# Kernel optimization log

Measured on AMD Instinct MI355X. Metric: run time of the kernel, lower is better.

## Reference

```python
import jax, jax.numpy as jnp
import numpy as np

N, C, H = 4096, 1024, 16
HD = C // H            # 64
DR = HD // 8           # 8 rope freqs per spatial axis


def setup_inputs() -> dict:
    key = jax.random.key(0)
    k1, k2, k3, k4, k5, k6 = jax.random.split(key, 6)
    x = jax.random.normal(k1, (N, C), dtype=jnp.float32)
    coords = jax.random.randint(k2, (N, 5), 0, 64, dtype=jnp.int32)  # [batch, t, h, w, z]
    w_qkv = jax.random.normal(k3, (3 * C, C), dtype=jnp.float32) / np.sqrt(C)
    w_out = jax.random.normal(k4, (C, C), dtype=jnp.float32) / np.sqrt(C)
    gamma_q = jnp.ones((H, HD), dtype=jnp.float32)
    gamma_k = jnp.ones((H, HD), dtype=jnp.float32)
    return {"x": x, "coords": coords, "w_qkv": w_qkv, "w_out": w_out,
            "gamma_q": gamma_q, "gamma_k": gamma_k}


def _rms_norm(t, gamma):
    # F.normalize(dim=-1) * gamma * sqrt(head_dim), computed in fp32
    t = t.astype(jnp.float32)
    nrm = jnp.linalg.norm(t, axis=-1, keepdims=True)
    return t / jnp.maximum(nrm, 1e-12) * gamma * np.float32(np.sqrt(HD))


def _rope_angles(coords):
    # freqs = 1/10000^(arange(DR)/HD); angles per axis (t,h,w,z), concat -> [N, 4*DR] = [N, HD/2]
    freqs = 1.0 / (10000.0 ** (jnp.arange(DR, dtype=jnp.float32) / HD))
    pos = coords[:, 1:].astype(jnp.float32)  # [N,4]
    ang = pos[:, :, None] * freqs[None, None, :]  # [N,4,DR]
    return ang.reshape(ang.shape[0], -1)  # [N, HD/2]


def _apply_rope(t, cos, sin):
    # t: [N,H,HD]; pairs (2i, 2i+1) rotated by angle[i]
    t2 = t.astype(jnp.float32).reshape(t.shape[0], t.shape[1], -1, 2)
    re = t2[..., 0] * cos - t2[..., 1] * sin
    im = t2[..., 0] * sin + t2[..., 1] * cos
    return jnp.stack([re, im], axis=-1).reshape(t.shape)


def reference(x, coords, w_qkv, w_out, gamma_q, gamma_k):
    n = x.shape[0]
    qkv = (x @ w_qkv.T).reshape(n, 3, H, HD)
    q, k, v = qkv[:, 0], qkv[:, 1], qkv[:, 2]  # [N,H,HD]
    q = _rms_norm(q, gamma_q)
    k = _rms_norm(k, gamma_k)
    ang = _rope_angles(coords)              # [N, HD/2]
    cos = jnp.cos(ang)[:, None, :]          # [N,1,HD/2] (broadcast over heads)
    sin = jnp.sin(ang)[:, None, :]
    q = _apply_rope(q, cos, sin)
    k = _apply_rope(k, cos, sin)
    scale = np.float32(1.0 / np.sqrt(HD))
    scores = jnp.einsum('nhd,mhd->hnm', q, k) * scale  # [H,N,N]
    attn = jax.nn.softmax(scores, axis=-1)
    out = jnp.einsum('hnm,mhd->nhd', attn, v).reshape(n, C)
    return out @ w_out.T
```

## Files before the change

### kernel.cpp

```cpp
#include <hip/hip_runtime.h>
#include <hip/hip_bf16.h>

typedef _Float16 half8 __attribute__((ext_vector_type(8)));
typedef _Float16 half4v __attribute__((ext_vector_type(4)));
typedef _Float16 half2 __attribute__((ext_vector_type(2)));
typedef float f32x4 __attribute__((ext_vector_type(4)));

constexpr int NT = 4096;
constexpr int CH = 1024;
constexpr int NH = 16;
constexpr int HD = 64;
constexpr int C3 = 3072;

#if __has_builtin(__builtin_amdgcn_exp2f)
#define EXP2(x) __builtin_amdgcn_exp2f(x)
#else
#define EXP2(x) exp2f(x)
#endif

#define GLOAD_LDS16(gp, lp) __builtin_amdgcn_global_load_lds( \
    (const __attribute__((address_space(1))) void*)(gp),      \
    (__attribute__((address_space(3))) void*)(lp), 16, 0, 0)

static __device__ inline half2 pk_f16(float a, float b) {
  auto r = __builtin_amdgcn_cvt_pkrtz(a, b);
  return *(half2*)&r;
}

__global__ __launch_bounds__(256) void cvt_kernel(const float* __restrict__ in,
                                                  _Float16* __restrict__ out, int n4) {
  int i = blockIdx.x * 256 + threadIdx.x;
  if (i >= n4) return;
  float4 v = ((const float4*)in)[i];
  half4v h;
  h[0] = (_Float16)v.x; h[1] = (_Float16)v.y; h[2] = (_Float16)v.z; h[3] = (_Float16)v.w;
  ((half4v*)out)[i] = h;
}

template <typename OutT>
__global__ __launch_bounds__(256) void gemm_bt(const _Float16* __restrict__ A,
                                               const _Float16* __restrict__ Bt,
                                               OutT* __restrict__ Cc,
                                               int M, int Nn, int K) {
  __shared__ _Float16 As[128][32];
  __shared__ _Float16 Bs[128][32];
  const int tid = threadIdx.x;
  const int lane = tid & 63, w = tid >> 6;
  const int l15 = lane & 15, l4 = lane >> 4;
  const int m0 = blockIdx.x * 128, n0 = blockIdx.y * 128;
  const int wr = w >> 1, wc = w & 1;
  const int rb = w * 32;
  const int rl = lane >> 2;
  const int cb = (lane & 3) * 8;
  f32x4 acc[4][4] = {};
  for (int k0 = 0; k0 < K; k0 += 32) {
    __syncthreads();
    GLOAD_LDS16(A  + (size_t)(m0 + rb + rl) * K + k0 + cb,      &As[rb][0]);
    GLOAD_LDS16(A  + (size_t)(m0 + rb + 16 + rl) * K + k0 + cb, &As[rb + 16][0]);
    GLOAD_LDS16(Bt + (size_t)(n0 + rb + rl) * K + k0 + cb,      &Bs[rb][0]);
    GLOAD_LDS16(Bt + (size_t)(n0 + rb + 16 + rl) * K + k0 + cb, &Bs[rb + 16][0]);
    __syncthreads();
    half8 af[4], bf[4];
#pragma unroll
    for (int mt = 0; mt < 4; ++mt) af[mt] = *(half8*)&As[wr * 64 + mt * 16 + l15][l4 * 8];
#pragma unroll
    for (int nt = 0; nt < 4; ++nt) bf[nt] = *(half8*)&Bs[wc * 64 + nt * 16 + l15][l4 * 8];
#pragma unroll
    for (int mt = 0; mt < 4; ++mt)
#pragma unroll
      for (int nt = 0; nt < 4; ++nt)
        acc[mt][nt] = __builtin_amdgcn_mfma_f32_16x16x32_f16(af[mt], bf[nt], acc[mt][nt], 0, 0, 0);
  }
#pragma unroll
  for (int mt = 0; mt < 4; ++mt)
#pragma unroll
    for (int nt = 0; nt < 4; ++nt)
#pragma unroll
      for (int r = 0; r < 4; ++r) {
        int row = m0 + wr * 64 + mt * 16 + l4 * 4 + r;
        int col = n0 + wc * 64 + nt * 16 + l15;
        Cc[(size_t)row * Nn + col] = (OutT)acc[mt][nt][r];
      }
}

__global__ __launch_bounds__(256) void rmsrope_kernel(const _Float16* __restrict__ qkv,
                                                      const int* __restrict__ coords,
                                                      const float* __restrict__ gq,
                                                      const float* __restrict__ gk,
                                                      _Float16* __restrict__ Qh,
                                                      _Float16* __restrict__ KF) {
  int gw = blockIdx.x * 4 + (threadIdx.x >> 6);
  int lane = threadIdx.x & 63;
  int n = gw >> 4, h = gw & 15;
  float q = (float)qkv[(size_t)n * C3 + h * HD + lane];
  float k = (float)qkv[(size_t)n * C3 + CH + h * HD + lane];
  float sq = q * q, sk = k * k;
#pragma unroll
  for (int m = 1; m < 64; m <<= 1) { sq += __shfl_xor(sq, m); sk += __shfl_xor(sk, m); }
  q *= 8.0f / fmaxf(sqrtf(sq), 1e-12f) * gq[h * HD + lane];
  k *= 8.0f / fmaxf(sqrtf(sk), 1e-12f) * gk[h * HD + lane];
  int j = lane >> 1, p = j >> 3, dr = j & 7;
  float ang = (float)coords[n * 5 + 1 + p] * __expf(-(float)dr * 0.14391157f);
  float cs = cosf(ang), sn = sinf(ang);
  float qp = __shfl_xor(q, 1), kp = __shfl_xor(k, 1);
  float qr, kr;
  if ((lane & 1) == 0) { qr = q * cs - qp * sn; kr = k * cs - kp * sn; }
  else                 { qr = qp * sn + q * cs; kr = kp * sn + k * cs; }
  Qh[((size_t)h * NT + n) * HD + lane] = (_Float16)(qr * 0.18033688f);
  int m64 = n & 63, kb = n >> 6;
  int t   = 2 * (m64 >> 5) + ((m64 >> 2) & 1);
  int i15 = 4 * ((m64 >> 3) & 3) + (m64 & 3);
  int kk = lane >> 5, ll4 = (lane >> 3) & 3, jj = lane & 7;
  KF[(size_t)h * NT * HD + (size_t)kb * 4096 +
     (size_t)(((t * 2 + kk) * 64 + ll4 * 16 + i15) * 8 + jj)] = (_Float16)kr;
}

__global__ __launch_bounds__(256) void vtrans_kernel(const _Float16* __restrict__ qkv,
                                                     _Float16* __restrict__ VF) {
  __shared__ _Float16 L[64][72];
  int h = blockIdx.y, n0 = blockIdx.x * 64, kb = blockIdx.x, t0 = threadIdx.x;
#pragma unroll
  for (int i = 0; i < 2; ++i) {
    int cid = t0 + i * 256, r = cid >> 3, c = cid & 7;
    *(half8*)&L[r][c * 8] = *(const half8*)(qkv + (size_t)(n0 + r) * C3 + 2 * CH + h * HD + c * 8);
  }
  __syncthreads();
#pragma unroll
  for (int i = 0; i < 2; ++i) {
    int cid = t0 + i * 256, d = cid >> 3, c = cid & 7;
    half8 v;
#pragma unroll
    for (int jj = 0; jj < 8; ++jj) v[jj] = L[c * 8 + jj][d];
    size_t flat = (size_t)h * NT * HD + (size_t)kb * 4096 +
                  (size_t)((((d >> 4) * 2 + (c >> 2)) * 64 + (c & 3) * 16 + (d & 15)) * 8);
    *(half8*)(VF + flat) = v;
  }
}

__global__ __launch_bounds__(256, 2) void attn_kernel(const _Float16* __restrict__ Qh,
                                                      const _Float16* __restrict__ KF,
                                                      const _Float16* __restrict__ VF,
                                                      _Float16* __restrict__ Oh) {
  const int tid = threadIdx.x, lane = tid & 63, w = tid >> 6;
  const int l15 = lane & 15, l4 = lane >> 4;
  int bid = blockIdx.x;
  int s = bid >> 3;
  int h = (bid & 7) * 2 + (s >> 5);
  int n0 = (s & 31) * 128;
  half8 qf[2][2];
#pragma unroll
  for (int qb = 0; qb < 2; ++qb)
#pragma unroll
    for (int kk = 0; kk < 2; ++kk)
      qf[qb][kk] = *(const half8*)(Qh + ((size_t)h * NT + n0 + w * 32 + qb * 16 + l15) * HD + kk * 32 + l4 * 8);
  f32x4 acc[2][4] = {};
  f32x4 acc5[2] = {};
  half8 of1 = {};
  if (l15 == 0) {
#pragma unroll
    for (int jq = 0; jq < 8; ++jq) of1[jq] = (_Float16)1.0f;
  }
  const _Float16* KFb = KF + (size_t)h * NT * HD + lane * 8;
  const _Float16* VFb = VF + (size_t)h * NT * HD + lane * 8;
  half8 kA[8], vA[8], kB[8], vB[8];
  auto loadset = [&](int kb, half8 (&k)[8], half8 (&v)[8]) {
    const _Float16* kp = KFb + (size_t)kb * 4096;
    const _Float16* vp = VFb + (size_t)kb * 4096;
#pragma unroll
    for (int f = 0; f < 8; ++f) {
      k[f] = *(const half8*)(kp + f * 512);
      v[f] = *(const half8*)(vp + f * 512);
    }
  };
  auto compute = [&](half8 (&k)[8], half8 (&v)[8]) {
    f32x4 sv[2][4] = {};
    __builtin_amdgcn_s_setprio(1);
#pragma unroll
    for (int t = 0; t < 4; ++t)
#pragma unroll
      for (int kk = 0; kk < 2; ++kk) {
        sv[0][t] = __builtin_amdgcn_mfma_f32_16x16x32_f16(k[t * 2 + kk], qf[0][kk], sv[0][t], 0, 0, 0);
        sv[1][t] = __builtin_amdgcn_mfma_f32_16x16x32_f16(k[t * 2 + kk], qf[1][kk], sv[1][t], 0, 0, 0);
      }
    __builtin_amdgcn_s_setprio(0);
    union U { half8 v; half2 p[4]; };
    U u[2][2];
#pragma unroll
    for (int qb = 0; qb < 2; ++qb) {
      float e[4][4];
#pragma unroll
      for (int t = 0; t < 4; ++t)
#pragma unroll
        for (int r = 0; r < 4; ++r) e[t][r] = EXP2(sv[qb][t][r]);
      u[qb][0].p[0] = pk_f16(e[0][0], e[0][1]); u[qb][0].p[1] = pk_f16(e[0][2], e[0][3]);
      u[qb][0].p[2] = pk_f16(e[1][0], e[1][1]); u[qb][0].p[3] = pk_f16(e[1][2], e[1][3]);
      u[qb][1].p[0] = pk_f16(e[2][0], e[2][1]); u[qb][1].p[1] = pk_f16(e[2][2], e[2][3]);
      u[qb][1].p[2] = pk_f16(e[3][0], e[3][1]); u[qb][1].p[3] = pk_f16(e[3][2], e[3][3]);
    }
    __builtin_amdgcn_s_setprio(1);
#pragma unroll
    for (int t = 0; t < 4; ++t)
#pragma unroll
      for (int kk = 0; kk < 2; ++kk) {
        acc[0][t] = __builtin_amdgcn_mfma_f32_16x16x32_f16(u[0][kk].v, v[t * 2 + kk], acc[0][t], 0, 0, 0);
        acc[1][t] = __builtin_amdgcn_mfma_f32_16x16x32_f16(u[1][kk].v, v[t * 2 + kk], acc[1][t], 0, 0, 0);
      }
    acc5[0] = __builtin_amdgcn_mfma_f32_16x16x32_f16(u[0][0].v, of1, acc5[0], 0, 0, 0);
    acc5[0] = __builtin_amdgcn_mfma_f32_16x16x32_f16(u[0][1].v, of1, acc5[0], 0, 0, 0);
    acc5[1] = __builtin_amdgcn_mfma_f32_16x16x32_f16(u[1][0].v, of1, acc5[1], 0, 0, 0);
    acc5[1] = __builtin_amdgcn_mfma_f32_16x16x32_f16(u[1][1].v, of1, acc5[1], 0, 0, 0);
    __builtin_amdgcn_s_setprio(0);
  };
  loadset(0, kA, vA);
  for (int kb = 0; kb < 64; kb += 2) {
    loadset(kb + 1, kB, vB);
    compute(kA, vA);
    if (kb + 2 < 64) loadset(kb + 2, kA, vA);
    compute(kB, vB);
  }
#pragma unroll
  for (int qb = 0; qb < 2; ++qb) {
    float linv[4];
#pragma unroll
    for (int r = 0; r < 4; ++r) linv[r] = 1.0f / __shfl(acc5[qb][r], lane & 48);
#pragma unroll
    for (int t = 0; t < 4; ++t)
#pragma unroll
      for (int r = 0; r < 4; ++r) {
        int row = n0 + w * 32 + qb * 16 + l4 * 4 + r;
        Oh[(size_t)row * CH + h * HD + t * 16 + l15] = (_Float16)(acc[qb][t][r] * linv[r]);
      }
  }
}

extern "C" void kernel_launch(void* const* d_in, const int* in_sizes, int n_in,
                              void* d_out, int out_size, void* d_ws, size_t ws_size,
                              hipStream_t stream) {
  const float* x      = (const float*)d_in[0];
  const int*   coords = (const int*)d_in[1];
  const float* w_qkv  = (const float*)d_in[2];
  const float* w_out  = (const float*)d_in[3];
  const float* gq     = (const float*)d_in[4];
  const float* gk     = (const float*)d_in[5];
  float* out = (float*)d_out;

  char* ws = (char*)d_ws;
  size_t off = 0;
  auto alloc = [&](size_t bytes) { char* p = ws + off; off += bytes; return p; };
  _Float16* xh   = (_Float16*)alloc((size_t)NT * CH * 2);
  _Float16* wqh  = (_Float16*)alloc((size_t)C3 * CH * 2);
  _Float16* woh  = (_Float16*)alloc((size_t)CH * CH * 2);
  _Float16* qkvh = (_Float16*)alloc((size_t)NT * C3 * 2);
  _Float16* Qh   = (_Float16*)alloc((size_t)NT * CH * 2);
  _Float16* KFh  = (_Float16*)alloc((size_t)NT * CH * 2);
  _Float16* VFh  = (_Float16*)alloc((size_t)NT * CH * 2);
  _Float16* Oh   = (_Float16*)alloc((size_t)NT * CH * 2);
  if (off > ws_size) return;

  cvt_kernel<<<NT * CH / 4 / 256, 256, 0, stream>>>(x, xh, NT * CH / 4);
  cvt_kernel<<<C3 * CH / 4 / 256, 256, 0, stream>>>(w_qkv, wqh, C3 * CH / 4);
  cvt_kernel<<<CH * CH / 4 / 256, 256, 0, stream>>>(w_out, woh, CH * CH / 4);
  gemm_bt<_Float16><<<dim3(NT / 128, C3 / 128), 256, 0, stream>>>(xh, wqh, qkvh, NT, C3, CH);
  rmsrope_kernel<<<NT * NH / 4, 256, 0, stream>>>(qkvh, coords, gq, gk, Qh, KFh);
  vtrans_kernel<<<dim3(NT / 64, NH), 256, 0, stream>>>(qkvh, VFh);
  attn_kernel<<<NH * (NT / 128), 256, 0, stream>>>(Qh, KFh, VFh, Oh);
  gemm_bt<float><<<dim3(NT / 128, CH / 128), 256, 0, stream>>>(Oh, woh, out, NT, CH, CH);
}
```

Before: 186.2 us.

## Stage K/V tiles through triple-buffered LDS and software-pipeline QK with softmax/PV

Replaces per-wave direct global loads of K/V fragments into registers with block-cooperative global_load_lds into a three-slot shared-memory ring. Each of the four waves now loads only a quarter of every tile instead of all of it. The loop is also software-pipelined so block kb's QK^T runs alongside block kb-1's softmax and PV, and the setprio hints are dropped. This is meant to cut redundant global traffic across waves and hide latency. In exchange it adds a barrier per iteration, LDS reads, and 48KB of LDS that may limit occupancy.

```diff
diff --git a/kernel.cpp b/kernel.cpp
--- a/kernel.cpp
+++ b/kernel.cpp
@@ -141,6 +141,8 @@
                                                       const _Float16* __restrict__ KF,
                                                       const _Float16* __restrict__ VF,
                                                       _Float16* __restrict__ Oh) {
+  __shared__ _Float16 KB[3][4096];
+  __shared__ _Float16 VB[3][4096];
   const int tid = threadIdx.x, lane = tid & 63, w = tid >> 6;
   const int l15 = lane & 15, l4 = lane >> 4;
   int bid = blockIdx.x;
@@ -160,31 +162,30 @@
 #pragma unroll
     for (int jq = 0; jq < 8; ++jq) of1[jq] = (_Float16)1.0f;
   }
-  const _Float16* KFb = KF + (size_t)h * NT * HD + lane * 8;
-  const _Float16* VFb = VF + (size_t)h * NT * HD + lane * 8;
-  half8 kA[8], vA[8], kB[8], vB[8];
-  auto loadset = [&](int kb, half8 (&k)[8], half8 (&v)[8]) {
-    const _Float16* kp = KFb + (size_t)kb * 4096;
-    const _Float16* vp = VFb + (size_t)kb * 4096;
-#pragma unroll
-    for (int f = 0; f < 8; ++f) {
-      k[f] = *(const half8*)(kp + f * 512);
-      v[f] = *(const half8*)(vp + f * 512);
+  const _Float16* KFh = KF + (size_t)h * NT * HD;
+  const _Float16* VFh = VF + (size_t)h * NT * HD;
+  auto stage = [&](int kb, int b) {
+    size_t g0 = (size_t)kb * 4096 + w * 512 + lane * 8;
+#pragma unroll
+    for (int cch = 0; cch < 2; ++cch) {
+      GLOAD_LDS16(KFh + g0 + cch * 2048, &KB[b][cch * 2048 + w * 512]);
+      GLOAD_LDS16(VFh + g0 + cch * 2048, &VB[b][cch * 2048 + w * 512]);
     }
   };
-  auto compute = [&](half8 (&k)[8], half8 (&v)[8]) {
-    f32x4 sv[2][4] = {};
-    __builtin_amdgcn_s_setprio(1);
+  auto qk = [&](int b, f32x4 (&sv)[2][4]) {
+    half8 kf[8];
+#pragma unroll
+    for (int f = 0; f < 8; ++f) kf[f] = *(half8*)&KB[b][f * 512 + lane * 8];
 #pragma unroll
     for (int t = 0; t < 4; ++t)
 #pragma unroll
       for (int kk = 0; kk < 2; ++kk) {
-        sv[0][t] = __builtin_amdgcn_mfma_f32_16x16x32_f16(k[t * 2 + kk], qf[0][kk], sv[0][t], 0, 0, 0);
-        sv[1][t] = __builtin_amdgcn_mfma_f32_16x16x32_f16(k[t * 2 + kk], qf[1][kk], sv[1][t], 0, 0, 0);
-      }
-    __builtin_amdgcn_s_setprio(0);
-    union U { half8 v; half2 p[4]; };
-    U u[2][2];
+        sv[0][t] = __builtin_amdgcn_mfma_f32_16x16x32_f16(kf[t * 2 + kk], qf[0][kk], sv[0][t], 0, 0, 0);
+        sv[1][t] = __builtin_amdgcn_mfma_f32_16x16x32_f16(kf[t * 2 + kk], qf[1][kk], sv[1][t], 0, 0, 0);
+      }
+  };
+  union U { half8 v; half2 p[4]; };
+  auto sm = [&](f32x4 (&sv)[2][4], U (&u)[2][2]) {
 #pragma unroll
     for (int qb = 0; qb < 2; ++qb) {
       float e[4][4];
@@ -197,27 +198,48 @@
       u[qb][1].p[0] = pk_f16(e[2][0], e[2][1]); u[qb][1].p[1] = pk_f16(e[2][2], e[2][3]);
       u[qb][1].p[2] = pk_f16(e[3][0], e[3][1]); u[qb][1].p[3] = pk_f16(e[3][2], e[3][3]);
     }
-    __builtin_amdgcn_s_setprio(1);
+  };
+  auto pv = [&](int b, U (&u)[2][2]) {
+    half8 vf[8];
+#pragma unroll
+    for (int f = 0; f < 8; ++f) vf[f] = *(half8*)&VB[b][f * 512 + lane * 8];
 #pragma unroll
     for (int t = 0; t < 4; ++t)
 #pragma unroll
       for (int kk = 0; kk < 2; ++kk) {
-        acc[0][t] = __builtin_amdgcn_mfma_f32_16x16x32_f16(u[0][kk].v, v[t * 2 + kk], acc[0][t], 0, 0, 0);
-        acc[1][t] = __builtin_amdgcn_mfma_f32_16x16x32_f16(u[1][kk].v, v[t * 2 + kk], acc[1][t], 0, 0, 0);
+        acc[0][t] = __builtin_amdgcn_mfma_f32_16x16x32_f16(u[0][kk].v, vf[t * 2 + kk], acc[0][t], 0, 0, 0);
+        acc[1][t] = __builtin_amdgcn_mfma_f32_16x16x32_f16(u[1][kk].v, vf[t * 2 + kk], acc[1][t], 0, 0, 0);
       }
     acc5[0] = __builtin_amdgcn_mfma_f32_16x16x32_f16(u[0][0].v, of1, acc5[0], 0, 0, 0);
     acc5[0] = __builtin_amdgcn_mfma_f32_16x16x32_f16(u[0][1].v, of1, acc5[0], 0, 0, 0);
     acc5[1] = __builtin_amdgcn_mfma_f32_16x16x32_f16(u[1][0].v, of1, acc5[1], 0, 0, 0);
     acc5[1] = __builtin_amdgcn_mfma_f32_16x16x32_f16(u[1][1].v, of1, acc5[1], 0, 0, 0);
-    __builtin_amdgcn_s_setprio(0);
-  };
-  loadset(0, kA, vA);
-  for (int kb = 0; kb < 64; kb += 2) {
-    loadset(kb + 1, kB, vB);
-    compute(kA, vA);
-    if (kb + 2 < 64) loadset(kb + 2, kA, vA);
-    compute(kB, vB);
-  }
+  };
+  f32x4 svA[2][4] = {}, svB[2][4] = {};
+  U uA[2][2], uB[2][2];
+  stage(0, 0);
+  __syncthreads();
+  stage(1, 1);
+  qk(0, svA);
+  for (int kb = 1; kb < 64; ++kb) {
+    int bc = kb % 3, bp = (kb - 1) % 3, bn = (kb + 1) % 3;
+    __syncthreads();
+    if (kb + 1 < 64) stage(kb + 1, bn);
+    if (kb & 1) {
+      qk(bc, svB); sm(svA, uA); pv(bp, uA);
+#pragma unroll
+      for (int qb = 0; qb < 2; ++qb)
+#pragma unroll
+        for (int t = 0; t < 4; ++t) svA[qb][t] = (f32x4){0.f, 0.f, 0.f, 0.f};
+    } else {
+      qk(bc, svA); sm(svB, uB); pv(bp, uB);
+#pragma unroll
+      for (int qb = 0; qb < 2; ++qb)
+#pragma unroll
+        for (int t = 0; t < 4; ++t) svB[qb][t] = (f32x4){0.f, 0.f, 0.f, 0.f};
+    }
+  }
+  sm(svB, uB); pv(0, uB);
 #pragma unroll
   for (int qb = 0; qb < 2; ++qb) {
     float linv[4];
```

After: 195.5 us. 1.05x slower.

## Stage K/V tiles through shared LDS instead of per-wave register loads

Applied to the files above, without the earlier changes.

Each block now loads every K/V tile once into shared memory with global_load_lds, split across the four waves, and each wave reads its fragments from LDS. Before, every wave loaded all K/V fragments from global memory straight into registers with register double-buffering. This cuts redundant global and L2 traffic by four and frees many VGPRs. The cost is the loss of software prefetch overlap: the single-buffered loop waits on two barriers per tile, so load latency is exposed.

```diff
diff --git a/kernel.cpp b/kernel.cpp
--- a/kernel.cpp
+++ b/kernel.cpp
@@ -141,6 +141,8 @@
                                                       const _Float16* __restrict__ KF,
                                                       const _Float16* __restrict__ VF,
                                                       _Float16* __restrict__ Oh) {
+  __shared__ _Float16 KB[4096];
+  __shared__ _Float16 VB[4096];
   const int tid = threadIdx.x, lane = tid & 63, w = tid >> 6;
   const int l15 = lane & 15, l4 = lane >> 4;
   int bid = blockIdx.x;
@@ -160,30 +162,30 @@
 #pragma unroll
     for (int jq = 0; jq < 8; ++jq) of1[jq] = (_Float16)1.0f;
   }
-  const _Float16* KFb = KF + (size_t)h * NT * HD + lane * 8;
-  const _Float16* VFb = VF + (size_t)h * NT * HD + lane * 8;
-  half8 kA[8], vA[8], kB[8], vB[8];
-  auto loadset = [&](int kb, half8 (&k)[8], half8 (&v)[8]) {
-    const _Float16* kp = KFb + (size_t)kb * 4096;
-    const _Float16* vp = VFb + (size_t)kb * 4096;
-#pragma unroll
-    for (int f = 0; f < 8; ++f) {
-      k[f] = *(const half8*)(kp + f * 512);
-      v[f] = *(const half8*)(vp + f * 512);
+  const _Float16* KFh = KF + (size_t)h * NT * HD + w * 512 + lane * 8;
+  const _Float16* VFh = VF + (size_t)h * NT * HD + w * 512 + lane * 8;
+  union U { half8 v; half2 p[4]; };
+  for (int kb = 0; kb < 64; ++kb) {
+    __syncthreads();
+    {
+      size_t g0 = (size_t)kb * 4096;
+      GLOAD_LDS16(KFh + g0,        &KB[w * 512]);
+      GLOAD_LDS16(KFh + g0 + 2048, &KB[2048 + w * 512]);
+      GLOAD_LDS16(VFh + g0,        &VB[w * 512]);
+      GLOAD_LDS16(VFh + g0 + 2048, &VB[2048 + w * 512]);
     }
-  };
-  auto compute = [&](half8 (&k)[8], half8 (&v)[8]) {
+    __syncthreads();
     f32x4 sv[2][4] = {};
     __builtin_amdgcn_s_setprio(1);
 #pragma unroll
     for (int t = 0; t < 4; ++t)
 #pragma unroll
       for (int kk = 0; kk < 2; ++kk) {
-        sv[0][t] = __builtin_amdgcn_mfma_f32_16x16x32_f16(k[t * 2 + kk], qf[0][kk], sv[0][t], 0, 0, 0);
-        sv[1][t] = __builtin_amdgcn_mfma_f32_16x16x32_f16(k[t * 2 + kk], qf[1][kk], sv[1][t], 0, 0, 0);
+        half8 kf = *(half8*)&KB[(t * 2 + kk) * 512 + lane * 8];
+        sv[0][t] = __builtin_amdgcn_mfma_f32_16x16x32_f16(kf, qf[0][kk], sv[0][t], 0, 0, 0);
+        sv[1][t] = __builtin_amdgcn_mfma_f32_16x16x32_f16(kf, qf[1][kk], sv[1][t], 0, 0, 0);
       }
     __builtin_amdgcn_s_setprio(0);
-    union U { half8 v; half2 p[4]; };
     U u[2][2];
 #pragma unroll
     for (int qb = 0; qb < 2; ++qb) {
@@ -202,21 +204,15 @@
     for (int t = 0; t < 4; ++t)
 #pragma unroll
       for (int kk = 0; kk < 2; ++kk) {
-        acc[0][t] = __builtin_amdgcn_mfma_f32_16x16x32_f16(u[0][kk].v, v[t * 2 + kk], acc[0][t], 0, 0, 0);
-        acc[1][t] = __builtin_amdgcn_mfma_f32_16x16x32_f16(u[1][kk].v, v[t * 2 + kk], acc[1][t], 0, 0, 0);
+        half8 vf = *(half8*)&VB[(t * 2 + kk) * 512 + lane * 8];
+        acc[0][t] = __builtin_amdgcn_mfma_f32_16x16x32_f16(u[0][kk].v, vf, acc[0][t], 0, 0, 0);
+        acc[1][t] = __builtin_amdgcn_mfma_f32_16x16x32_f16(u[1][kk].v, vf, acc[1][t], 0, 0, 0);
       }
     acc5[0] = __builtin_amdgcn_mfma_f32_16x16x32_f16(u[0][0].v, of1, acc5[0], 0, 0, 0);
     acc5[0] = __builtin_amdgcn_mfma_f32_16x16x32_f16(u[0][1].v, of1, acc5[0], 0, 0, 0);
     acc5[1] = __builtin_amdgcn_mfma_f32_16x16x32_f16(u[1][0].v, of1, acc5[1], 0, 0, 0);
     acc5[1] = __builtin_amdgcn_mfma_f32_16x16x32_f16(u[1][1].v, of1, acc5[1], 0, 0, 0);
     __builtin_amdgcn_s_setprio(0);
-  };
-  loadset(0, kA, vA);
-  for (int kb = 0; kb < 64; kb += 2) {
-    loadset(kb + 1, kB, vB);
-    compute(kA, vA);
-    if (kb + 2 < 64) loadset(kb + 2, kA, vA);
-    compute(kB, vB);
   }
 #pragma unroll
   for (int qb = 0; qb < 2; ++qb) {
```

New measurement: 178.9 us. -3.9%, faster.
